# Performance work log

Measured on AMD Instinct MI355X. Metric: run time of the kernel, lower is better.

The kernel has to match this reference:

```python
import jax, jax.numpy as jnp
import numpy as np

DIM = 1024
DFF = 4096
LN_EPS = 1e-5


def _layernorm(x, g, b):
    mu = jnp.mean(x, axis=-1, keepdims=True)
    var = jnp.mean((x - mu) ** 2, axis=-1, keepdims=True)
    return (x - mu) * jax.lax.rsqrt(var + LN_EPS) * g + b


def setup_inputs() -> dict:
    key = jax.random.key(0)
    ks = jax.random.split(key, 16)
    B, L, D, F = 4, 2048, DIM, DFF
    return {
        "x": jax.random.normal(ks[0], (B, L, D), dtype=jnp.float32),
        "hidden_real": jax.random.normal(ks[1], (B, D), dtype=jnp.float32),
        "hidden_imag": jax.random.normal(ks[2], (B, D), dtype=jnp.float32),
        # SConvLayer params (real/imag pairs, mirroring torch.view_as_real storage)
        "phazor_init": jax.random.normal(ks[3], (D, 2), dtype=jnp.float32),
        "phazor": jax.random.normal(ks[4], (D, 2), dtype=jnp.float32),
        # fc (gate) linear
        "fc_w": jax.random.normal(ks[5], (D, D), dtype=jnp.float32) / np.sqrt(D),
        "fc_b": jax.random.normal(ks[6], (D,), dtype=jnp.float32) * 0.01,
        # FFN
        "w1": jax.random.normal(ks[7], (F, D), dtype=jnp.float32) / np.sqrt(D),
        "b1": jax.random.normal(ks[8], (F,), dtype=jnp.float32) * 0.01,
        "w2": jax.random.normal(ks[9], (D, F), dtype=jnp.float32) / np.sqrt(F),
        "b2": jax.random.normal(ks[10], (D,), dtype=jnp.float32) * 0.01,
        # shared LayerNorm (used twice in the block with the same params)
        "ln_g": jnp.ones((D,), dtype=jnp.float32),
        "ln_b": jnp.zeros((D,), dtype=jnp.float32),
    }


def reference(x, hidden_real, hidden_imag, phazor_init, phazor,
              fc_w, fc_b, w1, b1, w2, b2, ln_g, ln_b):
    B, L, D = x.shape
    hidden = (hidden_real + 1j * hidden_imag).astype(jnp.complex64)

    x_res = x
    xn = _layernorm(x, ln_g, ln_b)

    # --- SConvLayer ---
    pz = (phazor[:, 0] + 1j * phazor[:, 1]).astype(jnp.complex64)  # [D]
    # magnitude exp(-|z|^2), phase = angle(z)
    p = jnp.exp(-(pz.real ** 2 + pz.imag ** 2)) * jnp.exp(1j * jnp.angle(pz))
    t = jnp.arange(L)
    prog = p[None, :] ** t[:, None]                      # [L, D] complex
    init_c = (phazor_init[:, 0] + 1j * phazor_init[:, 1]).astype(jnp.complex64)
    filt = prog * init_c[None, :]                        # [L, D]
    n2 = 2 * L
    filt_fft = jnp.fft.fft(filt, n=n2, axis=0)           # [2L, D]
    x_fft = jnp.fft.fft(xn.astype(jnp.complex64), n=n2, axis=1)  # [B, 2L, D]
    conv = jnp.fft.ifft(filt_fft[None] * x_fft, axis=1)[:, :L]   # [B, L, D]
    conv_with_past = conv + hidden[:, None, :] * prog[None] * p[None, None, :]
    sx = conv_with_past.real

    # --- gate ---
    y = jax.nn.silu(jnp.einsum('bld,ed->ble', x_res, fc_w) + fc_b)
    x2 = sx * y + x_res

    # --- FFN (same LayerNorm params) ---
    x3 = _layernorm(x2, ln_g, ln_b)
    h = jax.nn.silu(jnp.einsum('bld,fd->blf', x3, w1) + b1)
    out = jnp.einsum('blf,df->bld', h, w2) + b2 + x2
    return out, conv_with_past
```

## Files before the change

### kernel.cpp

```cpp
#include <hip/hip_runtime.h>
#include <hip/hip_bf16.h>

#define D_MODEL 1024
#define D_FF    4096
#define SEQ_LEN 2048
#define NBATCH  4
#define NROWS   (NBATCH*SEQ_LEN)
#define NCHUNK  32
#define CHUNK_L (SEQ_LEN/NCHUNK)
#define LN_EPS  1e-5f

typedef __hip_bfloat16 bf16;
typedef __attribute__((ext_vector_type(8))) short bf16x8;
typedef __attribute__((ext_vector_type(4))) float f32x4;

__device__ __forceinline__ void gload16(const bf16* g, bf16* l) {
    __builtin_amdgcn_global_load_lds(
        (const __attribute__((address_space(1))) void*)g,
        (__attribute__((address_space(3))) void*)l, 16, 0, 0);
}

__global__ void cast4(const float4* __restrict__ in, ushort4* __restrict__ out, int n4) {
    int i = blockIdx.x * blockDim.x + threadIdx.x;
    if (i < n4) {
        float4 v = in[i];
        union { ushort4 u; bf16 b[4]; } cv;
        cv.b[0] = __float2bfloat16(v.x); cv.b[1] = __float2bfloat16(v.y);
        cv.b[2] = __float2bfloat16(v.z); cv.b[3] = __float2bfloat16(v.w);
        out[i] = cv.u;
    }
}

__global__ void compute_pvec(const float* __restrict__ phz, float* __restrict__ pv) {
    int d = blockIdx.x * blockDim.x + threadIdx.x;
    if (d >= D_MODEL) return;
    float re = phz[2*d], im = phz[2*d+1];
    float r2 = re*re + im*im;
    float mag = expf(-r2);
    float pr, pim;
    if (r2 > 0.f) { float inv = mag / sqrtf(r2); pr = re*inv; pim = im*inv; }
    else          { pr = mag; pim = 0.f; }
    float ar = pr, ai = pim;
    #pragma unroll
    for (int i = 0; i < 6; i++) { float nr = ar*ar - ai*ai; float ni = 2.f*ar*ai; ar = nr; ai = ni; }
    pv[d]            = pr;
    pv[D_MODEL+d]    = pim;
    pv[2*D_MODEL+d]  = ar;
    pv[3*D_MODEL+d]  = ai;
}

__global__ __launch_bounds__(256) void ln_fused(const float* __restrict__ x,
                                                const float* __restrict__ g,
                                                const float* __restrict__ bta,
                                                float* __restrict__ outf,
                                                bf16*  __restrict__ outb,
                                                bf16*  __restrict__ rawb)
{
    int row = blockIdx.x;
    int tid = threadIdx.x;
    const float4* xr = (const float4*)(x + (size_t)row * D_MODEL);
    float4 v = xr[tid];
    if (rawb) {
        union { ushort4 u; bf16 b[4]; } cv;
        cv.b[0]=__float2bfloat16(v.x); cv.b[1]=__float2bfloat16(v.y);
        cv.b[2]=__float2bfloat16(v.z); cv.b[3]=__float2bfloat16(v.w);
        ((ushort4*)(rawb + (size_t)row * D_MODEL))[tid] = cv.u;
    }
    float s  = v.x + v.y + v.z + v.w;
    float s2 = v.x*v.x + v.y*v.y + v.z*v.z + v.w*v.w;
    for (int off = 32; off; off >>= 1) { s += __shfl_down(s, off); s2 += __shfl_down(s2, off); }
    __shared__ float red[8];
    int wid = tid >> 6, lane = tid & 63;
    if (lane == 0) { red[wid] = s; red[4+wid] = s2; }
    __syncthreads();
    if (tid == 0) {
        red[0] = red[0]+red[1]+red[2]+red[3];
        red[4] = red[4]+red[5]+red[6]+red[7];
    }
    __syncthreads();
    float mu  = red[0] * (1.f/D_MODEL);
    float var = red[4] * (1.f/D_MODEL) - mu*mu;
    float rstd = rsqrtf(var + LN_EPS);
    float4 gv = ((const float4*)g)[tid];
    float4 bv = ((const float4*)bta)[tid];
    float4 o;
    o.x = (v.x-mu)*rstd*gv.x + bv.x;
    o.y = (v.y-mu)*rstd*gv.y + bv.y;
    o.z = (v.z-mu)*rstd*gv.z + bv.z;
    o.w = (v.w-mu)*rstd*gv.w + bv.w;
    if (outf) ((float4*)(outf + (size_t)row * D_MODEL))[tid] = o;
    if (outb) {
        union { ushort4 u; bf16 b[4]; } cv;
        cv.b[0]=__float2bfloat16(o.x); cv.b[1]=__float2bfloat16(o.y);
        cv.b[2]=__float2bfloat16(o.z); cv.b[3]=__float2bfloat16(o.w);
        ((ushort4*)(outb + (size_t)row * D_MODEL))[tid] = cv.u;
    }
}

__global__ __launch_bounds__(256) void gate_ln(const float* __restrict__ cwp, int cstride,
                                               const bf16*  __restrict__ y,
                                               const float* __restrict__ x,
                                               const float* __restrict__ g,
                                               const float* __restrict__ bta,
                                               float* __restrict__ x2,
                                               bf16*  __restrict__ x3b)
{
    int row = blockIdx.x;
    int tid = threadIdx.x;
    size_t base = (size_t)row * D_MODEL + tid*4;
    float4 xv = *(const float4*)(x + base);
    union { ushort4 u; bf16 b[4]; } yv;
    yv.u = *(const ushort4*)(y + base);
    float4 cw;
    if (cstride == 1) {
        cw = *(const float4*)(cwp + base);
    } else {
        const float2* cp = (const float2*)cwp + base;
        cw.x = cp[0].x; cw.y = cp[1].x; cw.z = cp[2].x; cw.w = cp[3].x;
    }
    float4 v;
    v.x = cw.x * __bfloat162float(yv.b[0]) + xv.x;
    v.y = cw.y * __bfloat162float(yv.b[1]) + xv.y;
    v.z = cw.z * __bfloat162float(yv.b[2]) + xv.z;
    v.w = cw.w * __bfloat162float(yv.b[3]) + xv.w;
    *(float4*)(x2 + base) = v;

    float s  = v.x + v.y + v.z + v.w;
    float s2 = v.x*v.x + v.y*v.y + v.z*v.z + v.w*v.w;
    for (int off = 32; off; off >>= 1) { s += __shfl_down(s, off); s2 += __shfl_down(s2, off); }
    __shared__ float red[8];
    int wid = tid >> 6, lane = tid & 63;
    if (lane == 0) { red[wid] = s; red[4+wid] = s2; }
    __syncthreads();
    if (tid == 0) {
        red[0] = red[0]+red[1]+red[2]+red[3];
        red[4] = red[4]+red[5]+red[6]+red[7];
    }
    __syncthreads();
    float mu  = red[0] * (1.f/D_MODEL);
    float var = red[4] * (1.f/D_MODEL) - mu*mu;
    float rstd = rsqrtf(var + LN_EPS);
    float4 gv = ((const float4*)g)[tid];
    float4 bv = ((const float4*)bta)[tid];
    union { ushort4 u; bf16 b[4]; } cv;
    cv.b[0] = __float2bfloat16((v.x-mu)*rstd*gv.x + bv.x);
    cv.b[1] = __float2bfloat16((v.y-mu)*rstd*gv.y + bv.y);
    cv.b[2] = __float2bfloat16((v.z-mu)*rstd*gv.z + bv.z);
    cv.b[3] = __float2bfloat16((v.w-mu)*rstd*gv.w + bv.w);
    *(ushort4*)(x3b + base) = cv.u;
}

__global__ __launch_bounds__(256) void scan_pass1(const float* __restrict__ xn,
                                                  const float* __restrict__ pv,
                                                  const float* __restrict__ pini,
                                                  float* __restrict__ Sc)
{
    int d = blockIdx.x * 256 + threadIdx.x;
    int c = blockIdx.y, b = blockIdx.z;
    float pr = pv[d], pim = pv[D_MODEL+d];
    float icr = pini[2*d], ici = pini[2*d+1];
    float Sr = 0.f, Si = 0.f;
    const float* xp = xn + ((size_t)b*SEQ_LEN + c*CHUNK_L) * D_MODEL + d;
    #pragma unroll 8
    for (int i = 0; i < CHUNK_L; i++) {
        float xv = xp[(size_t)i * D_MODEL];
        float nr = pr*Sr - pim*Si + icr*xv;
        float ni = pr*Si + pim*Sr + ici*xv;
        Sr = nr; Si = ni;
    }
    size_t o = ((size_t)b*NCHUNK + c) * D_MODEL + d;
    Sc[2*o] = Sr; Sc[2*o+1] = Si;
}

__global__ __launch_bounds__(256) void scan_prefix(const float* __restrict__ Sc,
                                                   const float* __restrict__ pv,
                                                   const float* __restrict__ hr,
                                                   const float* __restrict__ hi,
                                                   float* __restrict__ pref)
{
    int d = blockIdx.x * 256 + threadIdx.x;
    int b = blockIdx.y;
    float qr = pv[2*D_MODEL+d], qi = pv[3*D_MODEL+d];
    float Ur = hr[b*D_MODEL+d], Ui = hi[b*D_MODEL+d];
    for (int c = 0; c < NCHUNK; c++) {
        size_t o = ((size_t)b*NCHUNK + c) * D_MODEL + d;
        pref[2*o] = Ur; pref[2*o+1] = Ui;
        float sr = Sc[2*o], si = Sc[2*o+1];
        float nr = qr*Ur - qi*Ui + sr;
        float ni = qr*Ui + qi*Ur + si;
        Ur = nr; Ui = ni;
    }
}

__global__ __launch_bounds__(256) void scan_pass2(const float* __restrict__ xn,
                                                  const float* __restrict__ pv,
                                                  const float* __restrict__ pini,
                                                  const float* __restrict__ pref,
                                                  float* __restrict__ cwp,
                                                  int interleaved)
{
    int d = blockIdx.x * 256 + threadIdx.x;
    int c = blockIdx.y, b = blockIdx.z;
    float pr = pv[d], pim = pv[D_MODEL+d];
    float icr = pini[2*d], ici = pini[2*d+1];
    size_t po = ((size_t)b*NCHUNK + c) * D_MODEL + d;
    float Ur = pref[2*po], Ui = pref[2*po+1];
    size_t base = ((size_t)b*SEQ_LEN + c*CHUNK_L) * D_MODEL + d;
    const float* xp = xn + base;
    if (interleaved) {
        float2* cp = (float2*)cwp + base;
        #pragma unroll 8
        for (int i = 0; i < CHUNK_L; i++) {
            float xv = xp[(size_t)i * D_MODEL];
            float nr = pr*Ur - pim*Ui + icr*xv;
            float ni = pr*Ui + pim*Ur + ici*xv;
            Ur = nr; Ui = ni;
            cp[(size_t)i * D_MODEL] = make_float2(Ur, Ui);
        }
    } else {
        float* cp = cwp + base;
        #pragma unroll 8
        for (int i = 0; i < CHUNK_L; i++) {
            float xv = xp[(size_t)i * D_MODEL];
            float nr = pr*Ur - pim*Ui + icr*xv;
            float ni = pr*Ui + pim*Ur + ici*xv;
            Ur = nr; Ui = ni;
            cp[(size_t)i * D_MODEL] = Ur;
        }
    }
}

template<int EPI>
__device__ __forceinline__ void epi_store(float v, size_t idx,
                                          const float* e0, int e0_stride, const float* e1,
                                          float* outf, bf16* outb)
{
    if (EPI == 1) {
        float yv = v / (1.f + __expf(-v));
        outb[idx] = __float2bfloat16(yv);
    } else {
        outf[idx] = v + e0[idx];
    }
}

#define BM 128
#define BN 128
#define BK 32

template<int EPI>
__global__ __launch_bounds__(256) void gemm_bt(const bf16* __restrict__ A,
                                               const bf16* __restrict__ Bt,
                                               const float* __restrict__ bias,
                                               const float* __restrict__ e0, int e0_stride,
                                               const float* __restrict__ e1,
                                               float* __restrict__ outf,
                                               bf16*  __restrict__ outb,
                                               int M, int N, int K)
{
    __shared__ __align__(16) bf16 As[3][BM*BK];
    __shared__ __align__(16) bf16 Bs[3][BM*BK];
    int tid = threadIdx.x;
    int m0 = blockIdx.x * BM;
    int n0 = blockIdx.y * BN;

    int wid = tid >> 6, lane = tid & 63;
    int wm = (wid >> 1) * 64, wn = (wid & 1) * 64;
    int lr = lane & 15;
    int lkc = lane >> 4;

    int rl = lane >> 2;
    int cS = (lane & 3) ^ ((rl >> 1) & 3);
    const bf16* gA0 = A  + (size_t)(m0 +      wid*16 + rl) * K + cS*8;
    const bf16* gA1 = A  + (size_t)(m0 + 64 + wid*16 + rl) * K + cS*8;
    const bf16* gB0 = Bt + (size_t)(n0 +      wid*16 + rl) * K + cS*8;
    const bf16* gB1 = Bt + (size_t)(n0 + 64 + wid*16 + rl) * K + cS*8;
    int lo0 = (     wid*16) * BK;
    int lo1 = (64 + wid*16) * BK;

    int keyr = (lr >> 1) & 3;
    int cR = (lkc ^ keyr) * 8;
    int offA[4], offB[4];
    #pragma unroll
    for (int i = 0; i < 4; i++) {
        offA[i] = (wm + i*16 + lr) * BK + cR;
        offB[i] = (wn + i*16 + lr) * BK + cR;
    }

    int nt = K / BK;
    auto stage = [&](int slot, int tile) {
        int k0 = tile * BK;
        gload16(gA0 + k0, &As[slot][lo0]);
        gload16(gA1 + k0, &As[slot][lo1]);
        gload16(gB0 + k0, &Bs[slot][lo0]);
        gload16(gB1 + k0, &Bs[slot][lo1]);
    };
    f32x4 acc[4][4] = {};
    auto compute = [&](int slot) {
        bf16x8 af[4], bfv[4];
        #pragma unroll
        for (int i = 0; i < 4; i++) {
            af[i]  = *(const bf16x8*)&As[slot][offA[i]];
            bfv[i] = *(const bf16x8*)&Bs[slot][offB[i]];
        }
        #pragma unroll
        for (int i = 0; i < 4; i++)
            #pragma unroll
            for (int j = 0; j < 4; j++)
                acc[i][j] = __builtin_amdgcn_mfma_f32_16x16x32_bf16(af[i], bfv[j], acc[i][j], 0, 0, 0);
    };

    stage(0, 0); stage(1, 1); stage(2, 2);

    int s = 0;
    for (int t = 0; t < nt - 3; ++t) {
        asm volatile("s_waitcnt vmcnt(8)" ::: "memory");
        __builtin_amdgcn_s_barrier();
        __builtin_amdgcn_sched_barrier(0);
        compute(s);
        asm volatile("" ::: "memory");
        __builtin_amdgcn_s_barrier();
        stage(s, t + 3);
        s = (s == 2) ? 0 : s + 1;
    }
    asm volatile("s_waitcnt vmcnt(8)" ::: "memory");
    __builtin_amdgcn_s_barrier();
    __builtin_amdgcn_sched_barrier(0);
    compute(s);
    s = (s == 2) ? 0 : s + 1;
    asm volatile("s_waitcnt vmcnt(4)" ::: "memory");
    __builtin_amdgcn_s_barrier();
    __builtin_amdgcn_sched_barrier(0);
    compute(s);
    s = (s == 2) ? 0 : s + 1;
    asm volatile("s_waitcnt vmcnt(0)" ::: "memory");
    __builtin_amdgcn_s_barrier();
    __builtin_amdgcn_sched_barrier(0);
    compute(s);

    int mrow = 4 * (lane >> 4);
    #pragma unroll
    for (int i = 0; i < 4; i++) {
        #pragma unroll
        for (int j = 0; j < 4; j++) {
            int nb = n0 + wn + j*16 + lr;
            float bb = bias[nb];
            #pragma unroll
            for (int r = 0; r < 4; r++) {
                int m = m0 + wm + i*16 + mrow + r;
                size_t idx = (size_t)m * N + nb;
                epi_store<EPI>(acc[i][j][r] + bb, idx, e0, e0_stride, e1, outf, outb);
            }
        }
    }
}

#define TM 256
#define TN 256

template<int EPI>
__global__ __launch_bounds__(512, 2) void gemm256(const bf16* __restrict__ A,
                                                  const bf16* __restrict__ Bt,
                                                  const float* __restrict__ bias,
                                                  const float* __restrict__ e0, int e0_stride,
                                                  const float* __restrict__ e1,
                                                  float* __restrict__ outf,
                                                  bf16*  __restrict__ outb,
                                                  int M, int N, int K)
{
    __shared__ __align__(16) bf16 As[2][TM*BK];
    __shared__ __align__(16) bf16 Bs[2][TN*BK];
    int tid = threadIdx.x;
    int m0 = blockIdx.x * TM;
    int n0 = blockIdx.y * TN;

    int wid = tid >> 6, lane = tid & 63;
    int wr = wid >> 2, wc = wid & 3;
    int wm = wr * 128, wn = wc * 64;
    int lr = lane & 15;
    int lkc = lane >> 4;

    int rl = tid >> 2;
    int cS = (tid & 3) ^ ((rl >> 1) & 3);
    const bf16* gA0 = A  + (size_t)(m0 +       rl) * K + cS*8;
    const bf16* gA1 = A  + (size_t)(m0 + 128 + rl) * K + cS*8;
    const bf16* gB0 = Bt + (size_t)(n0 +       rl) * K + cS*8;
    const bf16* gB1 = Bt + (size_t)(n0 + 128 + rl) * K + cS*8;
    int lo0 = (      wid*16) * BK;
    int lo1 = (128 + wid*16) * BK;

    int keyr = (lr >> 1) & 3;
    int cR = (lkc ^ keyr) * 8;
    int offA[8], offB[4];
    #pragma unroll
    for (int i = 0; i < 8; i++) offA[i] = (wm + i*16 + lr) * BK + cR;
    #pragma unroll
    for (int j = 0; j < 4; j++) offB[j] = (wn + j*16 + lr) * BK + cR;

    int nt = K / BK;
    auto stage = [&](int slot, int tile) {
        int k0 = tile * BK;
        gload16(gA0 + k0, &As[slot][lo0]);
        gload16(gA1 + k0, &As[slot][lo1]);
        gload16(gB0 + k0, &Bs[slot][lo0]);
        gload16(gB1 + k0, &Bs[slot][lo1]);
    };
    f32x4 acc[8][4] = {};
    auto compute = [&](int slot) {
        bf16x8 af[8], bfv[4];
        #pragma unroll
        for (int i = 0; i < 8; i++) af[i]  = *(const bf16x8*)&As[slot][offA[i]];
        #pragma unroll
        for (int j = 0; j < 4; j++) bfv[j] = *(const bf16x8*)&Bs[slot][offB[j]];
        #pragma unroll
        for (int i = 0; i < 8; i++)
            #pragma unroll
            for (int j = 0; j < 4; j++)
                acc[i][j] = __builtin_amdgcn_mfma_f32_16x16x32_bf16(af[i], bfv[j], acc[i][j], 0, 0, 0);
    };

    stage(0, 0); stage(1, 1);

    int s = 0;
    for (int t = 0; t < nt - 2; ++t) {
        asm volatile("s_waitcnt vmcnt(4)" ::: "memory");
        __builtin_amdgcn_s_barrier();
        __builtin_amdgcn_sched_barrier(0);
        compute(s);
        asm volatile("" ::: "memory");
        __builtin_amdgcn_s_barrier();
        stage(s, t + 2);
        s ^= 1;
    }
    asm volatile("s_waitcnt vmcnt(4)" ::: "memory");
    __builtin_amdgcn_s_barrier();
    __builtin_amdgcn_sched_barrier(0);
    compute(s);
    s ^= 1;
    asm volatile("s_waitcnt vmcnt(0)" ::: "memory");
    __builtin_amdgcn_s_barrier();
    __builtin_amdgcn_sched_barrier(0);
    compute(s);

    int mrow = 4 * (lane >> 4);
    #pragma unroll
    for (int i = 0; i < 8; i++) {
        #pragma unroll
        for (int j = 0; j < 4; j++) {
            int nb = n0 + wn + j*16 + lr;
            float bb = bias[nb];
            #pragma unroll
            for (int r = 0; r < 4; r++) {
                int m = m0 + wm + i*16 + mrow + r;
                size_t idx = (size_t)m * N + nb;
                epi_store<EPI>(acc[i][j][r] + bb, idx, e0, e0_stride, e1, outf, outb);
            }
        }
    }
}

extern "C" void kernel_launch(void* const* d_in, const int* in_sizes, int n_in,
                              void* d_out, int out_size, void* d_ws, size_t ws_size,
                              hipStream_t stream)
{
    const float* x    = (const float*)d_in[0];
    const float* hr   = (const float*)d_in[1];
    const float* hi   = (const float*)d_in[2];
    const float* pini = (const float*)d_in[3];
    const float* phz  = (const float*)d_in[4];
    const float* fcw  = (const float*)d_in[5];
    const float* fcb  = (const float*)d_in[6];
    const float* w1   = (const float*)d_in[7];
    const float* b1   = (const float*)d_in[8];
    const float* w2   = (const float*)d_in[9];
    const float* b2   = (const float*)d_in[10];
    const float* lng  = (const float*)d_in[11];
    const float* lnb  = (const float*)d_in[12];

    float* out = (float*)d_out;
    float* cwp = out + (size_t)NROWS * D_MODEL;
    int interleaved = (out_size >= NROWS * D_MODEL * 3) ? 1 : 0;

    char* ws = (char*)d_ws;
    size_t off = 0;
    bf16*  wfcb = (bf16*)(ws + off);  off += (size_t)D_MODEL*D_MODEL*2;
    bf16*  w1b  = (bf16*)(ws + off);  off += (size_t)D_FF*D_MODEL*2;
    bf16*  w2b  = (bf16*)(ws + off);  off += (size_t)D_MODEL*D_FF*2;
    float* pv   = (float*)(ws + off); off += (size_t)4*D_MODEL*4;
    float* xn   = (float*)(ws + off); off += (size_t)NROWS*D_MODEL*4;
    bf16*  xbf  = (bf16*)(ws + off);  off += (size_t)NROWS*D_MODEL*2;
    float* Sc   = (float*)(ws + off); off += (size_t)NBATCH*NCHUNK*D_MODEL*2*4;
    float* pref = (float*)(ws + off); off += (size_t)NBATCH*NCHUNK*D_MODEL*2*4;
    float* x2   = (float*)(ws + off); off += (size_t)NROWS*D_MODEL*4;
    bf16*  x3b  = (bf16*)(ws + off);  off += (size_t)NROWS*D_MODEL*2;
    bf16*  hbuf = (bf16*)(ws + off);  off += (size_t)NROWS*D_FF*2;
    bf16*  ybuf = (bf16*)(ws + off);  off += (size_t)NROWS*D_MODEL*2;

    cast4<<<1024, 256, 0, stream>>>((const float4*)fcw, (ushort4*)wfcb, D_MODEL*D_MODEL/4);
    cast4<<<4096, 256, 0, stream>>>((const float4*)w1,  (ushort4*)w1b,  D_FF*D_MODEL/4);
    cast4<<<4096, 256, 0, stream>>>((const float4*)w2,  (ushort4*)w2b,  D_MODEL*D_FF/4);

    compute_pvec<<<4, 256, 0, stream>>>(phz, pv);

    ln_fused<<<NROWS, 256, 0, stream>>>(x, lng, lnb, xn, nullptr, xbf);

    scan_pass1<<<dim3(4, NCHUNK, NBATCH), 256, 0, stream>>>(xn, pv, pini, Sc);
    scan_prefix<<<dim3(4, NBATCH), 256, 0, stream>>>(Sc, pv, hr, hi, pref);
    scan_pass2<<<dim3(4, NCHUNK, NBATCH), 256, 0, stream>>>(xn, pv, pini, pref, cwp, interleaved);

    gemm_bt<1><<<dim3(NROWS/BM, D_MODEL/BN), 256, 0, stream>>>(
        xbf, wfcb, fcb, nullptr, 1, nullptr, nullptr, ybuf, NROWS, D_MODEL, D_MODEL);

    gate_ln<<<NROWS, 256, 0, stream>>>(cwp, interleaved ? 2 : 1, ybuf, x, lng, lnb, x2, x3b);

    gemm256<1><<<dim3(NROWS/TM, D_FF/TN), 512, 0, stream>>>(
        x3b, w1b, b1, nullptr, 1, nullptr, nullptr, hbuf, NROWS, D_FF, D_MODEL);

    gemm_bt<2><<<dim3(NROWS/BM, D_MODEL/BN), 256, 0, stream>>>(
        hbuf, w2b, b2, x2, 1, nullptr, out, nullptr, NROWS, D_MODEL, D_FF);
}
```

Baseline: 294.7 us.

## Triple-buffer the 256x256 FFN-up GEMM with split A/B staging and ping-pong halves

Replaces the double-buffered 256x256 GEMM with a three-slot LDS pipeline. A and B tile loads are issued separately and staggered so each K-step's compute runs in two halves of 16 MFMAs, with loads for later tiles issued between them. Wave priority is raised around MFMA blocks to keep matrix units fed. This is meant to hide global-to-LDS latency better, at the cost of more LDS (three slots may lower occupancy from the two-block launch bound) and trickier vmcnt accounting.

```diff
diff --git a/kernel.cpp b/kernel.cpp
--- a/kernel.cpp
+++ b/kernel.cpp
@@ -358,17 +358,17 @@
 #define TN 256
 
 template<int EPI>
-__global__ __launch_bounds__(512, 2) void gemm256(const bf16* __restrict__ A,
-                                                  const bf16* __restrict__ Bt,
-                                                  const float* __restrict__ bias,
-                                                  const float* __restrict__ e0, int e0_stride,
-                                                  const float* __restrict__ e1,
-                                                  float* __restrict__ outf,
-                                                  bf16*  __restrict__ outb,
-                                                  int M, int N, int K)
-{
-    __shared__ __align__(16) bf16 As[2][TM*BK];
-    __shared__ __align__(16) bf16 Bs[2][TN*BK];
+__global__ __launch_bounds__(512, 2) void gemm256p(const bf16* __restrict__ A,
+                                                   const bf16* __restrict__ Bt,
+                                                   const float* __restrict__ bias,
+                                                   const float* __restrict__ e0, int e0_stride,
+                                                   const float* __restrict__ e1,
+                                                   float* __restrict__ outf,
+                                                   bf16*  __restrict__ outb,
+                                                   int M, int N, int K)
+{
+    __shared__ __align__(16) bf16 As[3][TM*BK];
+    __shared__ __align__(16) bf16 Bs[3][TN*BK];
     int tid = threadIdx.x;
     int m0 = blockIdx.x * TM;
     int n0 = blockIdx.y * TN;
@@ -379,14 +379,11 @@
     int lr = lane & 15;
     int lkc = lane >> 4;
 
-    int rl = tid >> 2;
-    int cS = (tid & 3) ^ ((rl >> 1) & 3);
-    const bf16* gA0 = A  + (size_t)(m0 +       rl) * K + cS*8;
-    const bf16* gA1 = A  + (size_t)(m0 + 128 + rl) * K + cS*8;
-    const bf16* gB0 = Bt + (size_t)(n0 +       rl) * K + cS*8;
-    const bf16* gB1 = Bt + (size_t)(n0 + 128 + rl) * K + cS*8;
-    int lo0 = (      wid*16) * BK;
-    int lo1 = (128 + wid*16) * BK;
+    int rs = tid >> 2;
+    int cS = (tid & 3) ^ ((rs >> 1) & 3);
+    const bf16* gA = A  + (size_t)m0 * K + cS*8;
+    const bf16* gB = Bt + (size_t)n0 * K + cS*8;
+    int ldst = tid * 8;
 
     int keyr = (lr >> 1) & 3;
     int cR = (lkc ^ keyr) * 8;
@@ -397,49 +394,61 @@
     for (int j = 0; j < 4; j++) offB[j] = (wn + j*16 + lr) * BK + cR;
 
     int nt = K / BK;
-    auto stage = [&](int slot, int tile) {
+    auto stA = [&](int slot, int tile) {
         int k0 = tile * BK;
-        gload16(gA0 + k0, &As[slot][lo0]);
-        gload16(gA1 + k0, &As[slot][lo1]);
-        gload16(gB0 + k0, &Bs[slot][lo0]);
-        gload16(gB1 + k0, &Bs[slot][lo1]);
+        gload16(gA + (size_t)rs * K + k0,         &As[slot][ldst]);
+        gload16(gA + (size_t)(128 + rs) * K + k0, &As[slot][4096 + ldst]);
     };
+    auto stB = [&](int slot, int tile) {
+        int k0 = tile * BK;
+        gload16(gB + (size_t)rs * K + k0,         &Bs[slot][ldst]);
+        gload16(gB + (size_t)(128 + rs) * K + k0, &Bs[slot][4096 + ldst]);
+    };
+
     f32x4 acc[8][4] = {};
-    auto compute = [&](int slot) {
-        bf16x8 af[8], bfv[4];
-        #pragma unroll
-        for (int i = 0; i < 8; i++) af[i]  = *(const bf16x8*)&As[slot][offA[i]];
-        #pragma unroll
-        for (int j = 0; j < 4; j++) bfv[j] = *(const bf16x8*)&Bs[slot][offB[j]];
-        #pragma unroll
-        for (int i = 0; i < 8; i++)
+    stA(0, 0); stB(0, 0); stA(1, 1); stB(1, 1); stB(2, 2);
+
+    int s = 0;
+    for (int t = 0; t < nt; ++t) {
+        int sA = (s >= 1) ? s - 1 : 2;
+        if (t < nt - 2)       { asm volatile("s_waitcnt vmcnt(6)" ::: "memory"); }
+        else if (t == nt - 2) { asm volatile("s_waitcnt vmcnt(4)" ::: "memory"); }
+        else                  { asm volatile("s_waitcnt vmcnt(0)" ::: "memory"); }
+        __builtin_amdgcn_s_barrier();
+        asm volatile("" ::: "memory");
+        bf16x8 af0[4], bfv[4];
+        #pragma unroll
+        for (int i = 0; i < 4; i++) af0[i] = *(const bf16x8*)&As[s][offA[i]];
+        #pragma unroll
+        for (int j = 0; j < 4; j++) bfv[j] = *(const bf16x8*)&Bs[s][offB[j]];
+        if (t + 2 < nt) stA(sA, t + 2);
+        asm volatile("s_waitcnt lgkmcnt(0)" ::: "memory");
+        __builtin_amdgcn_sched_barrier(0);
+        __builtin_amdgcn_s_setprio(1);
+        #pragma unroll
+        for (int i = 0; i < 4; i++)
             #pragma unroll
             for (int j = 0; j < 4; j++)
-                acc[i][j] = __builtin_amdgcn_mfma_f32_16x16x32_bf16(af[i], bfv[j], acc[i][j], 0, 0, 0);
-    };
-
-    stage(0, 0); stage(1, 1);
-
-    int s = 0;
-    for (int t = 0; t < nt - 2; ++t) {
-        asm volatile("s_waitcnt vmcnt(4)" ::: "memory");
+                acc[i][j] = __builtin_amdgcn_mfma_f32_16x16x32_bf16(af0[i], bfv[j], acc[i][j], 0, 0, 0);
+        __builtin_amdgcn_s_setprio(0);
         __builtin_amdgcn_s_barrier();
+        asm volatile("" ::: "memory");
+        bf16x8 af1[4];
+        #pragma unroll
+        for (int i = 0; i < 4; i++) af1[i] = *(const bf16x8*)&As[s][offA[4+i]];
+        if (t + 3 < nt) stB(s, t + 3);
+        asm volatile("s_waitcnt lgkmcnt(0)" ::: "memory");
         __builtin_amdgcn_sched_barrier(0);
-        compute(s);
-        asm volatile("" ::: "memory");
-        __builtin_amdgcn_s_barrier();
-        stage(s, t + 2);
-        s ^= 1;
-    }
-    asm volatile("s_waitcnt vmcnt(4)" ::: "memory");
-    __builtin_amdgcn_s_barrier();
-    __builtin_amdgcn_sched_barrier(0);
-    compute(s);
-    s ^= 1;
+        __builtin_amdgcn_s_setprio(1);
+        #pragma unroll
+        for (int i = 0; i < 4; i++)
+            #pragma unroll
+            for (int j = 0; j < 4; j++)
+                acc[4+i][j] = __builtin_amdgcn_mfma_f32_16x16x32_bf16(af1[i], bfv[j], acc[4+i][j], 0, 0, 0);
+        __builtin_amdgcn_s_setprio(0);
+        s = (s == 2) ? 0 : s + 1;
+    }
     asm volatile("s_waitcnt vmcnt(0)" ::: "memory");
-    __builtin_amdgcn_s_barrier();
-    __builtin_amdgcn_sched_barrier(0);
-    compute(s);
 
     int mrow = 4 * (lane >> 4);
     #pragma unroll
@@ -512,7 +521,7 @@
 
     gate_ln<<<NROWS, 256, 0, stream>>>(cwp, interleaved ? 2 : 1, ybuf, x, lng, lnb, x2, x3b);
 
-    gemm256<1><<<dim3(NROWS/TM, D_FF/TN), 512, 0, stream>>>(
+    gemm256p<1><<<dim3(NROWS/TM, D_FF/TN), 512, 0, stream>>>(
         x3b, w1b, b1, nullptr, 1, nullptr, nullptr, hbuf, NROWS, D_FF, D_MODEL);
 
     gemm_bt<2><<<dim3(NROWS/BM, D_MODEL/BN), 256, 0, stream>>>(
```

Measured after the change: 280.7 us. 4.8% less time.
